# Performance work log

Hardware: AMD Instinct MI355X
Metric: run time of the kernel (lower is better)

The kernel has to match this reference:

```python
import jax, jax.numpy as jnp
import numpy as np

N_POINTS = 131072
N_SEG = 16
C = 256
BN_EPS = 1e-5


def setup_inputs() -> dict:
    key = jax.random.key(0)
    ks = jax.random.split(key, 6)
    x = jax.random.normal(ks[0], (N_POINTS, C), jnp.float32)
    # Ragged segment end-offsets (cumulative counts), strictly increasing, last == N_POINTS.
    rng = np.random.default_rng(0)
    base = N_POINTS // N_SEG
    counts = base + rng.integers(-base // 32, base // 32, N_SEG)
    counts[-1] += N_POINTS - counts.sum()
    o = jnp.asarray(np.cumsum(counts), jnp.int32)
    s1 = 1.0 / np.sqrt(2 * C)  # linear1: Linear(2C -> C)
    s2 = 1.0 / np.sqrt(C)      # linear2: Linear(C -> C)
    W1 = jax.random.uniform(ks[1], (2 * C, C), jnp.float32, -s1, s1)
    b1 = jax.random.uniform(ks[2], (C,), jnp.float32, -s1, s1)
    W2 = jax.random.uniform(ks[3], (C, C), jnp.float32, -s2, s2)
    b2 = jax.random.uniform(ks[4], (C,), jnp.float32, -s2, s2)
    gamma = jnp.ones((C,), jnp.float32)
    beta = jnp.zeros((C,), jnp.float32)
    return {"x": x, "o": o, "W1": W1, "b1": b1, "W2": W2, "b2": b2,
            "gamma": gamma, "beta": beta}


def reference(x, o, W1, b1, W2, b2, gamma, beta):
    n, c = x.shape
    s = o.shape[0]
    # segment id per point from cumulative end-offsets
    seg_id = jnp.searchsorted(o, jnp.arange(n), side="right")  # [N]
    counts = jnp.concatenate([o[:1], o[1:] - o[:-1]])          # [S]
    # per-segment mean pooling (x_b.sum(0, True) / cnt)
    sums = jax.ops.segment_sum(x, seg_id, num_segments=s)      # [S, C]
    means = sums / counts[:, None].astype(x.dtype)
    # linear2: Linear(C, C) + ReLU on segment means
    y = jax.nn.relu(means @ W2 + b2)                           # [S, C]
    # broadcast-concat back to points, then linear1: Linear(2C, C)
    h = jnp.concatenate([x, y[seg_id]], axis=1) @ W1 + b1      # [N, C]
    # BatchNorm1d (training mode: batch statistics, biased variance) + ReLU
    mu = h.mean(axis=0)
    var = h.var(axis=0)
    out = jax.nn.relu((h - mu) * (gamma / jnp.sqrt(var + BN_EPS)) + beta)
    return out
```

## Files before the change

### kernel.cpp

```cpp
#include <hip/hip_runtime.h>
#include <hip/hip_bf16.h>
#include <stdint.h>

#define N_PTS 131072
#define NC 256
#define NSEG 16
#define BN_EPSF 1e-5f

typedef __attribute__((ext_vector_type(8))) short bf16x8;
typedef __attribute__((ext_vector_type(4))) float f32x4;

__device__ __forceinline__ unsigned short f2bf(float f) {
  union { float f; uint32_t u; } v; v.f = f;
  uint32_t u = v.u;
  uint32_t r = (u + 0x7fffu + ((u >> 16) & 1u)) >> 16;
  return (unsigned short)r;
}
__device__ __forceinline__ float bf2f(unsigned short h) {
  union { uint32_t u; float f; } v; v.u = ((uint32_t)h) << 16; return v.f;
}

__global__ void k_zero(float* __restrict__ p, int n) {
  int i = blockIdx.x * 256 + threadIdx.x;
  if (i < n) p[i] = 0.f;
}

__global__ __launch_bounds__(256) void k_segsum_convert(
    const float* __restrict__ x, const int* __restrict__ o,
    unsigned short* __restrict__ x_bf, float* __restrict__ seg_sums) {
  __shared__ int o_s[NSEG];
  __shared__ float s_acc[2][NC];
  int t = threadIdx.x;
  if (t < NSEG) o_s[t] = o[t];
  s_acc[0][t] = 0.f;
  s_acc[1][t] = 0.f;
  __syncthreads();
  int g = t >> 6, l = t & 63;
  int row0 = blockIdx.x * 64;
  int c0 = l * 4;
  int s0 = 0;
  while (o_s[s0] <= row0) ++s0;
  int e0 = o_s[s0];
  int s1 = (s0 < NSEG - 1) ? s0 + 1 : s0;
  float4 accA = {0.f, 0.f, 0.f, 0.f}, accB = {0.f, 0.f, 0.f, 0.f};
  const float4* xv = (const float4*)x;
#pragma unroll
  for (int i = 0; i < 16; ++i) {
    int r = row0 + g + i * 4;
    float4 v = xv[(size_t)r * 64 + l];
    ushort4 b;
    b.x = f2bf(v.x); b.y = f2bf(v.y); b.z = f2bf(v.z); b.w = f2bf(v.w);
    *(ushort4*)(x_bf + (size_t)r * NC + c0) = b;
    bool inA = (r < e0);
    accA.x += inA ? v.x : 0.f; accB.x += inA ? 0.f : v.x;
    accA.y += inA ? v.y : 0.f; accB.y += inA ? 0.f : v.y;
    accA.z += inA ? v.z : 0.f; accB.z += inA ? 0.f : v.z;
    accA.w += inA ? v.w : 0.f; accB.w += inA ? 0.f : v.w;
  }
  atomicAdd(&s_acc[0][c0 + 0], accA.x);
  atomicAdd(&s_acc[0][c0 + 1], accA.y);
  atomicAdd(&s_acc[0][c0 + 2], accA.z);
  atomicAdd(&s_acc[0][c0 + 3], accA.w);
  atomicAdd(&s_acc[1][c0 + 0], accB.x);
  atomicAdd(&s_acc[1][c0 + 1], accB.y);
  atomicAdd(&s_acc[1][c0 + 2], accB.z);
  atomicAdd(&s_acc[1][c0 + 3], accB.w);
  __syncthreads();
  atomicAdd(&seg_sums[s0 * NC + t], s_acc[0][t]);
  atomicAdd(&seg_sums[s1 * NC + t], s_acc[1][t]);
}

__global__ __launch_bounds__(256) void k_w1t(const float* __restrict__ W1,
                                             unsigned short* __restrict__ w1t) {
  __shared__ float tile[64][65];
  int t = threadIdx.x;
  int bx = blockIdx.x & 3, by = blockIdx.x >> 2;
  int k0 = by * 64, j0 = bx * 64;
  int r = t >> 6, c = t & 63;
#pragma unroll
  for (int i = 0; i < 16; ++i) {
    int kk = r + i * 4;
    tile[kk][c] = W1[(size_t)(k0 + kk) * NC + j0 + c];
  }
  __syncthreads();
#pragma unroll
  for (int i = 0; i < 16; ++i) {
    int jj = r + i * 4;
    w1t[(size_t)(j0 + jj) * NC + k0 + c] = f2bf(tile[c][jj]);
  }
}

__global__ __launch_bounds__(256) void k_seg_mlp(
    const int* __restrict__ o, const float* __restrict__ seg_sums,
    const float* __restrict__ W1, const float* __restrict__ b1,
    const float* __restrict__ W2, const float* __restrict__ b2,
    float* __restrict__ z) {
  __shared__ float mean_s[NC];
  __shared__ float y_s[NC];
  int b = blockIdx.x, j = threadIdx.x;
  int start = (b == 0) ? 0 : o[b - 1];
  float inv = 1.f / (float)(o[b] - start);
  mean_s[j] = seg_sums[b * NC + j] * inv;
  __syncthreads();
  float a = b2[j];
  for (int k = 0; k < NC; ++k) a += mean_s[k] * W2[k * NC + j];
  y_s[j] = fmaxf(a, 0.f);
  __syncthreads();
  float a2 = b1[j];
  for (int k = 0; k < NC; ++k) a2 += y_s[k] * W1[(NC + k) * NC + j];
  z[b * NC + j] = a2;
}

__global__ __launch_bounds__(256) void k_gemm(
    const unsigned short* __restrict__ x_bf, const unsigned short* __restrict__ w1t,
    const int* __restrict__ o, const float* __restrict__ z,
    unsigned short* __restrict__ h_bf,
    float* __restrict__ colsum, float* __restrict__ colsumsq) {
  __shared__ __align__(16) unsigned short lA[128 * 32];
  __shared__ __align__(16) unsigned short lB[128 * 32];
  __shared__ float s_sum[128];
  __shared__ float s_sq[128];
  __shared__ int o_s[NSEG];

  int t = threadIdx.x;
  int lane = t & 63, w = t >> 6;
  int wr = w >> 1, wc = w & 1;
  int bid = blockIdx.x;
  int ct = bid & 1, rt = bid >> 1;
  const int row0 = rt * 128, colT = ct * 128;

  if (t < 128) { s_sum[t] = 0.f; s_sq[t] = 0.f; }
  if (t < NSEG) o_s[t] = o[t];

  f32x4 acc[4][4] = {};

  for (int kt = 0; kt < 8; ++kt) {
    {
      int c = t;
      const unsigned short* ga = x_bf + (size_t)(row0 + (c >> 2)) * NC + kt * 32 + (c & 3) * 8;
      __builtin_amdgcn_global_load_lds(
          (const __attribute__((address_space(1))) void*)ga,
          (__attribute__((address_space(3))) void*)(lA + c * 8), 16, 0, 0);
      const unsigned short* gb = w1t + (size_t)(colT + (c >> 2)) * NC + kt * 32 + (c & 3) * 8;
      __builtin_amdgcn_global_load_lds(
          (const __attribute__((address_space(1))) void*)gb,
          (__attribute__((address_space(3))) void*)(lB + c * 8), 16, 0, 0);
      c = t + 256;
      ga = x_bf + (size_t)(row0 + (c >> 2)) * NC + kt * 32 + (c & 3) * 8;
      __builtin_amdgcn_global_load_lds(
          (const __attribute__((address_space(1))) void*)ga,
          (__attribute__((address_space(3))) void*)(lA + c * 8), 16, 0, 0);
      gb = w1t + (size_t)(colT + (c >> 2)) * NC + kt * 32 + (c & 3) * 8;
      __builtin_amdgcn_global_load_lds(
          (const __attribute__((address_space(1))) void*)gb,
          (__attribute__((address_space(3))) void*)(lB + c * 8), 16, 0, 0);
    }
    __syncthreads();
    bf16x8 af[4], bf[4];
#pragma unroll
    for (int m = 0; m < 4; ++m)
      af[m] = *(const bf16x8*)(lA + (wr * 64 + m * 16 + (lane & 15)) * 32 + (lane >> 4) * 8);
#pragma unroll
    for (int n = 0; n < 4; ++n)
      bf[n] = *(const bf16x8*)(lB + (wc * 64 + n * 16 + (lane & 15)) * 32 + (lane >> 4) * 8);
#pragma unroll
    for (int m = 0; m < 4; ++m)
#pragma unroll
      for (int n = 0; n < 4; ++n)
        acc[m][n] = __builtin_amdgcn_mfma_f32_16x16x32_bf16(af[m], bf[n], acc[m][n], 0, 0, 0);
    __syncthreads();
  }

  int s0 = 0;
  while (o_s[s0] <= row0) ++s0;
  int e0 = o_s[s0];
  int s1 = (s0 < NSEG - 1) ? s0 + 1 : s0;
  int cl = lane & 15, q = lane >> 4;
#pragma unroll
  for (int n = 0; n < 4; ++n) {
    int col = colT + wc * 64 + n * 16 + cl;
    float zA = z[s0 * NC + col], zB = z[s1 * NC + col];
    float ps = 0.f, pq = 0.f;
#pragma unroll
    for (int m = 0; m < 4; ++m) {
      int rbase = row0 + wr * 64 + m * 16 + q * 4;
#pragma unroll
      for (int r = 0; r < 4; ++r) {
        int row = rbase + r;
        float hv = acc[m][n][r] + ((row < e0) ? zA : zB);
        h_bf[(size_t)row * NC + col] = f2bf(hv);
        ps += hv; pq += hv * hv;
      }
    }
    ps += __shfl_xor(ps, 16, 64); ps += __shfl_xor(ps, 32, 64);
    pq += __shfl_xor(pq, 16, 64); pq += __shfl_xor(pq, 32, 64);
    if (q == 0) {
      atomicAdd(&s_sum[wc * 64 + n * 16 + cl], ps);
      atomicAdd(&s_sq[wc * 64 + n * 16 + cl], pq);
    }
  }
  __syncthreads();
  if (t < 128) {
    atomicAdd(&colsum[colT + t], s_sum[t]);
    atomicAdd(&colsumsq[colT + t], s_sq[t]);
  }
}

__global__ void k_bn_final(const float* __restrict__ colsum, const float* __restrict__ colsumsq,
                           const float* __restrict__ gamma, const float* __restrict__ beta,
                           float* __restrict__ scale, float* __restrict__ shift) {
  int t = threadIdx.x;
  float invN = 1.f / (float)N_PTS;
  float mu = colsum[t] * invN;
  float var = colsumsq[t] * invN - mu * mu;
  float sc = gamma[t] * rsqrtf(var + BN_EPSF);
  scale[t] = sc;
  shift[t] = beta[t] - mu * sc;
}

__global__ __launch_bounds__(256) void k_bn_apply(
    const unsigned short* __restrict__ h_bf, const float* __restrict__ scale,
    const float* __restrict__ shift, float* __restrict__ out) {
  int t = threadIdx.x;
  size_t idx = (size_t)blockIdx.x * 256 + t;
  size_t l0 = idx * 4;
  int col = (int)(l0 & 255);
  uint2 hv = *(const uint2*)(h_bf + l0);
  float4 sc = *(const float4*)(scale + col);
  float4 sh = *(const float4*)(shift + col);
  float f0 = bf2f((unsigned short)(hv.x & 0xffffu));
  float f1 = bf2f((unsigned short)(hv.x >> 16));
  float f2 = bf2f((unsigned short)(hv.y & 0xffffu));
  float f3 = bf2f((unsigned short)(hv.y >> 16));
  float4 o0;
  o0.x = fmaxf(f0 * sc.x + sh.x, 0.f);
  o0.y = fmaxf(f1 * sc.y + sh.y, 0.f);
  o0.z = fmaxf(f2 * sc.z + sh.z, 0.f);
  o0.w = fmaxf(f3 * sc.w + sh.w, 0.f);
  *(float4*)(out + l0) = o0;
}

extern "C" void kernel_launch(void* const* d_in, const int* in_sizes, int n_in,
                              void* d_out, int out_size, void* d_ws, size_t ws_size,
                              hipStream_t stream) {
  const float* x = (const float*)d_in[0];
  const int* o = (const int*)d_in[1];
  const float* W1 = (const float*)d_in[2];
  const float* b1 = (const float*)d_in[3];
  const float* W2 = (const float*)d_in[4];
  const float* b2 = (const float*)d_in[5];
  const float* gamma = (const float*)d_in[6];
  const float* beta = (const float*)d_in[7];
  float* out = (float*)d_out;

  char* ws = (char*)d_ws;
  unsigned short* x_bf = (unsigned short*)ws;
  unsigned short* h_bf = (unsigned short*)(ws + 67108864);
  char* base2 = ws + 134217728;
  float* seg_sums = (float*)(base2);
  float* colsum   = (float*)(base2 + 16384);
  float* colsumsq = (float*)(base2 + 17408);
  float* z        = (float*)(base2 + 18432);
  float* scale    = (float*)(base2 + 34816);
  float* shift    = (float*)(base2 + 35840);
  unsigned short* w1t = (unsigned short*)(base2 + 36864);

  k_zero<<<18, 256, 0, stream>>>(seg_sums, 4608);
  k_segsum_convert<<<2048, 256, 0, stream>>>(x, o, x_bf, seg_sums);
  k_w1t<<<16, 256, 0, stream>>>(W1, w1t);
  k_seg_mlp<<<16, 256, 0, stream>>>(o, seg_sums, W1, b1, W2, b2, z);
  k_gemm<<<2048, 256, 0, stream>>>(x_bf, w1t, o, z, h_bf, colsum, colsumsq);
  k_bn_final<<<1, 256, 0, stream>>>(colsum, colsumsq, gamma, beta, scale, shift);
  k_bn_apply<<<32768, 256, 0, stream>>>(h_bf, scale, shift, out);
}
```

Measured before the change: 350.0 us.

## Fuse prep kernels, preload full W1 tile in LDS, read A from global, fold BN finalize

```diff
diff --git a/kernel.cpp b/kernel.cpp
--- a/kernel.cpp
+++ b/kernel.cpp
@@ -6,6 +6,7 @@
 #define NC 256
 #define NSEG 16
 #define BN_EPSF 1e-5f
+#define BJ 264
 
 typedef __attribute__((ext_vector_type(8))) short bf16x8;
 typedef __attribute__((ext_vector_type(4))) float f32x4;
@@ -20,9 +21,28 @@
   union { uint32_t u; float f; } v; v.u = ((uint32_t)h) << 16; return v.f;
 }
 
-__global__ void k_zero(float* __restrict__ p, int n) {
-  int i = blockIdx.x * 256 + threadIdx.x;
-  if (i < n) p[i] = 0.f;
+__global__ __launch_bounds__(256) void k_prep(const float* __restrict__ W1,
+                                              unsigned short* __restrict__ w1t,
+                                              float* __restrict__ stats) {
+  __shared__ float tile[64][65];
+  int t = threadIdx.x;
+  int b = blockIdx.x;
+  stats[b * 288 + t] = 0.f;
+  if (t < 32) stats[b * 288 + 256 + t] = 0.f;
+  int bx = b & 3, by = b >> 2;
+  int k0 = by * 64, j0 = bx * 64;
+  int r = t >> 6, c = t & 63;
+#pragma unroll
+  for (int i = 0; i < 16; ++i) {
+    int kk = r + i * 4;
+    tile[kk][c] = W1[(size_t)(k0 + kk) * NC + j0 + c];
+  }
+  __syncthreads();
+#pragma unroll
+  for (int i = 0; i < 16; ++i) {
+    int jj = r + i * 4;
+    w1t[(size_t)(j0 + jj) * NC + k0 + c] = f2bf(tile[c][jj]);
+  }
 }
 
 __global__ __launch_bounds__(256) void k_segsum_convert(
@@ -36,7 +56,7 @@
   s_acc[1][t] = 0.f;
   __syncthreads();
   int g = t >> 6, l = t & 63;
-  int row0 = blockIdx.x * 64;
+  int row0 = blockIdx.x * 128;
   int c0 = l * 4;
   int s0 = 0;
   while (o_s[s0] <= row0) ++s0;
@@ -45,7 +65,7 @@
   float4 accA = {0.f, 0.f, 0.f, 0.f}, accB = {0.f, 0.f, 0.f, 0.f};
   const float4* xv = (const float4*)x;
 #pragma unroll
-  for (int i = 0; i < 16; ++i) {
+  for (int i = 0; i < 32; ++i) {
     int r = row0 + g + i * 4;
     float4 v = xv[(size_t)r * 64 + l];
     ushort4 b;
@@ -68,26 +88,6 @@
   __syncthreads();
   atomicAdd(&seg_sums[s0 * NC + t], s_acc[0][t]);
   atomicAdd(&seg_sums[s1 * NC + t], s_acc[1][t]);
-}
-
-__global__ __launch_bounds__(256) void k_w1t(const float* __restrict__ W1,
-                                             unsigned short* __restrict__ w1t) {
-  __shared__ float tile[64][65];
-  int t = threadIdx.x;
-  int bx = blockIdx.x & 3, by = blockIdx.x >> 2;
-  int k0 = by * 64, j0 = bx * 64;
-  int r = t >> 6, c = t & 63;
-#pragma unroll
-  for (int i = 0; i < 16; ++i) {
-    int kk = r + i * 4;
-    tile[kk][c] = W1[(size_t)(k0 + kk) * NC + j0 + c];
-  }
-  __syncthreads();
-#pragma unroll
-  for (int i = 0; i < 16; ++i) {
-    int jj = r + i * 4;
-    w1t[(size_t)(j0 + jj) * NC + k0 + c] = f2bf(tile[c][jj]);
-  }
 }
 
 __global__ __launch_bounds__(256) void k_seg_mlp(
@@ -116,8 +116,7 @@
     const int* __restrict__ o, const float* __restrict__ z,
     unsigned short* __restrict__ h_bf,
     float* __restrict__ colsum, float* __restrict__ colsumsq) {
-  __shared__ __align__(16) unsigned short lA[128 * 32];
-  __shared__ __align__(16) unsigned short lB[128 * 32];
+  __shared__ __align__(16) unsigned short lB[128 * BJ];
   __shared__ float s_sum[128];
   __shared__ float s_sq[128];
   __shared__ int o_s[NSEG];
@@ -126,49 +125,43 @@
   int lane = t & 63, w = t >> 6;
   int wr = w >> 1, wc = w & 1;
   int bid = blockIdx.x;
-  int ct = bid & 1, rt = bid >> 1;
+  int rt = (bid & 7) | ((bid >> 4) << 3);
+  int ct = (bid >> 3) & 1;
   const int row0 = rt * 128, colT = ct * 128;
 
   if (t < 128) { s_sum[t] = 0.f; s_sq[t] = 0.f; }
   if (t < NSEG) o_s[t] = o[t];
 
+  {
+    const uint4* gsrc = (const uint4*)(w1t + (size_t)colT * NC);
+#pragma unroll
+    for (int i = 0; i < 16; ++i) {
+      int c = t + i * 256;
+      int j = c >> 5, kc = c & 31;
+      uint4 v = gsrc[j * 32 + kc];
+      *(uint4*)(lB + j * BJ + kc * 8) = v;
+    }
+  }
+  __syncthreads();
+
   f32x4 acc[4][4] = {};
-
+  const unsigned short* aBase =
+      x_bf + (size_t)(row0 + wr * 64 + (lane & 15)) * NC + (lane >> 4) * 8;
+  const unsigned short* bBase = lB + (wc * 64 + (lane & 15)) * BJ + (lane >> 4) * 8;
+#pragma unroll
   for (int kt = 0; kt < 8; ++kt) {
-    {
-      int c = t;
-      const unsigned short* ga = x_bf + (size_t)(row0 + (c >> 2)) * NC + kt * 32 + (c & 3) * 8;
-      __builtin_amdgcn_global_load_lds(
-          (const __attribute__((address_space(1))) void*)ga,
-          (__attribute__((address_space(3))) void*)(lA + c * 8), 16, 0, 0);
-      const unsigned short* gb = w1t + (size_t)(colT + (c >> 2)) * NC + kt * 32 + (c & 3) * 8;
-      __builtin_amdgcn_global_load_lds(
-          (const __attribute__((address_space(1))) void*)gb,
-          (__attribute__((address_space(3))) void*)(lB + c * 8), 16, 0, 0);
-      c = t + 256;
-      ga = x_bf + (size_t)(row0 + (c >> 2)) * NC + kt * 32 + (c & 3) * 8;
-      __builtin_amdgcn_global_load_lds(
-          (const __attribute__((address_space(1))) void*)ga,
-          (__attribute__((address_space(3))) void*)(lA + c * 8), 16, 0, 0);
-      gb = w1t + (size_t)(colT + (c >> 2)) * NC + kt * 32 + (c & 3) * 8;
-      __builtin_amdgcn_global_load_lds(
-          (const __attribute__((address_space(1))) void*)gb,
-          (__attribute__((address_space(3))) void*)(lB + c * 8), 16, 0, 0);
-    }
-    __syncthreads();
-    bf16x8 af[4], bf[4];
+    bf16x8 af[4], bfr[4];
 #pragma unroll
     for (int m = 0; m < 4; ++m)
-      af[m] = *(const bf16x8*)(lA + (wr * 64 + m * 16 + (lane & 15)) * 32 + (lane >> 4) * 8);
+      af[m] = *(const bf16x8*)(aBase + (size_t)m * 16 * NC + kt * 32);
 #pragma unroll
     for (int n = 0; n < 4; ++n)
-      bf[n] = *(const bf16x8*)(lB + (wc * 64 + n * 16 + (lane & 15)) * 32 + (lane >> 4) * 8);
+      bfr[n] = *(const bf16x8*)(bBase + n * 16 * BJ + kt * 32);
 #pragma unroll
     for (int m = 0; m < 4; ++m)
 #pragma unroll
       for (int n = 0; n < 4; ++n)
-        acc[m][n] = __builtin_amdgcn_mfma_f32_16x16x32_bf16(af[m], bf[n], acc[m][n], 0, 0, 0);
-    __syncthreads();
+        acc[m][n] = __builtin_amdgcn_mfma_f32_16x16x32_bf16(af[m], bfr[n], acc[m][n], 0, 0, 0);
   }
 
   int s0 = 0;
@@ -206,28 +199,33 @@
   }
 }
 
-__global__ void k_bn_final(const float* __restrict__ colsum, const float* __restrict__ colsumsq,
-                           const float* __restrict__ gamma, const float* __restrict__ beta,
-                           float* __restrict__ scale, float* __restrict__ shift) {
-  int t = threadIdx.x;
-  float invN = 1.f / (float)N_PTS;
-  float mu = colsum[t] * invN;
-  float var = colsumsq[t] * invN - mu * mu;
-  float sc = gamma[t] * rsqrtf(var + BN_EPSF);
-  scale[t] = sc;
-  shift[t] = beta[t] - mu * sc;
-}
-
 __global__ __launch_bounds__(256) void k_bn_apply(
-    const unsigned short* __restrict__ h_bf, const float* __restrict__ scale,
-    const float* __restrict__ shift, float* __restrict__ out) {
-  int t = threadIdx.x;
+    const unsigned short* __restrict__ h_bf,
+    const float* __restrict__ colsum, const float* __restrict__ colsumsq,
+    const float* __restrict__ gamma, const float* __restrict__ beta,
+    float* __restrict__ out) {
+  int t = threadIdx.x;
+  int c4 = t & 63;
+  float4 cs = ((const float4*)colsum)[c4];
+  float4 cq = ((const float4*)colsumsq)[c4];
+  float4 gm = ((const float4*)gamma)[c4];
+  float4 bt = ((const float4*)beta)[c4];
+  const float invN = 1.f / (float)N_PTS;
+  float4 sc, sh;
+  {
+    float mu, var;
+    mu = cs.x * invN; var = cq.x * invN - mu * mu;
+    sc.x = gm.x * rsqrtf(var + BN_EPSF); sh.x = bt.x - mu * sc.x;
+    mu = cs.y * invN; var = cq.y * invN - mu * mu;
+    sc.y = gm.y * rsqrtf(var + BN_EPSF); sh.y = bt.y - mu * sc.y;
+    mu = cs.z * invN; var = cq.z * invN - mu * mu;
+    sc.z = gm.z * rsqrtf(var + BN_EPSF); sh.z = bt.z - mu * sc.z;
+    mu = cs.w * invN; var = cq.w * invN - mu * mu;
+    sc.w = gm.w * rsqrtf(var + BN_EPSF); sh.w = bt.w - mu * sc.w;
+  }
   size_t idx = (size_t)blockIdx.x * 256 + t;
   size_t l0 = idx * 4;
-  int col = (int)(l0 & 255);
   uint2 hv = *(const uint2*)(h_bf + l0);
-  float4 sc = *(const float4*)(scale + col);
-  float4 sh = *(const float4*)(shift + col);
   float f0 = bf2f((unsigned short)(hv.x & 0xffffu));
   float f1 = bf2f((unsigned short)(hv.x >> 16));
   float f2 = bf2f((unsigned short)(hv.y & 0xffffu));
@@ -261,15 +259,11 @@
   float* colsum   = (float*)(base2 + 16384);
   float* colsumsq = (float*)(base2 + 17408);
   float* z        = (float*)(base2 + 18432);
-  float* scale    = (float*)(base2 + 34816);
-  float* shift    = (float*)(base2 + 35840);
   unsigned short* w1t = (unsigned short*)(base2 + 36864);
 
-  k_zero<<<18, 256, 0, stream>>>(seg_sums, 4608);
-  k_segsum_convert<<<2048, 256, 0, stream>>>(x, o, x_bf, seg_sums);
-  k_w1t<<<16, 256, 0, stream>>>(W1, w1t);
+  k_prep<<<16, 256, 0, stream>>>(W1, w1t, seg_sums);
+  k_segsum_convert<<<1024, 256, 0, stream>>>(x, o, x_bf, seg_sums);
   k_seg_mlp<<<16, 256, 0, stream>>>(o, seg_sums, W1, b1, W2, b2, z);
   k_gemm<<<2048, 256, 0, stream>>>(x_bf, w1t, o, z, h_bf, colsum, colsumsq);
-  k_bn_final<<<1, 256, 0, stream>>>(colsum, colsumsq, gamma, beta, scale, shift);
-  k_bn_apply<<<32768, 256, 0, stream>>>(h_bf, scale, shift, out);
-}
+  k_bn_apply<<<32768, 256, 0, stream>>>(h_bf, colsum, colsumsq, gamma, beta, out);
+}
```

Result: slower. 357.2 us (+2.1%).
